# Kernel optimization log

Measured on AMD Instinct MI355X. Metric: run time of the kernel, lower is better.

The kernel has to match this reference:

```python
import jax, jax.numpy as jnp
import numpy as np

B, N, K = 8, 2048, 64          # clouds, points per cloud, max neighbors
R1, R2 = 0.2, 0.4              # radii of the two SA modules
S1, S2 = N // 2, N // 8        # fps: ratio 0.5, then 0.25 of S1
DIMS1 = [3, 64, 64, 128]
DIMS2 = [128 + 3, 128, 128, 256]
DIMS3 = [256 + 3, 256, 512, 1024]


def _fps(pos, S):
    # farthest point sampling, deterministic start at index 0. pos: [N,3] -> [S] int32
    d = jnp.sum((pos - pos[0]) ** 2, axis=-1)
    sel0 = jnp.zeros((S,), jnp.int32)
    def body(i, carry):
        d, sel = carry
        nxt = jnp.argmax(d).astype(jnp.int32)
        sel = sel.at[i].set(nxt)
        d = jnp.minimum(d, jnp.sum((pos - pos[nxt]) ** 2, axis=-1))
        return d, sel
    _, sel = jax.lax.fori_loop(1, S, body, (d, sel0))
    return sel


def _radius(c_pos, pos, r, k):
    # up to k nearest points within radius r of each centroid.
    d2 = jnp.sum((c_pos[:, None, :] - pos[None, :, :]) ** 2, axis=-1)  # [M,N]
    score = jnp.where(d2 <= r * r, -d2, -jnp.inf)
    neg, idx = jax.lax.top_k(score, k)   # nearest-first
    mask = neg > -jnp.inf
    return idx, mask


def _mlp(h, params):
    # PyG MLP, plain_last=True; BatchNorm at default init is identity -> omitted.
    n = len(params)
    for i, (W, b) in enumerate(params):
        h = h @ W + b
        if i < n - 1:
            h = jax.nn.relu(h)
    return h


def _sa(x, pos, S, r, params):
    # SAModule: fps -> radius -> PointNetConv (gather, per-edge MLP, max-aggregate)
    idx = _fps(pos, S)
    c_pos = pos[idx]                                  # [S,3]
    nbr, mask = _radius(c_pos, pos, r, K)             # [S,K]
    rel = pos[nbr] - c_pos[:, None, :]                # [S,K,3]
    h = rel if x is None else jnp.concatenate([x[nbr], rel], axis=-1)
    h = _mlp(h, params)                               # [S,K,C]
    # each centroid always contains itself in its ball, so no empty groups
    h = jnp.where(mask[:, :, None], h, -jnp.inf).max(axis=1)
    return h, c_pos


def _make_mlp_params(key, dims):
    params = []
    for i in range(len(dims) - 1):
        key, k1 = jax.random.split(key)
        W = jax.random.normal(k1, (dims[i], dims[i + 1]), jnp.float32) * np.sqrt(2.0 / dims[i])
        b = jnp.zeros((dims[i + 1],), jnp.float32)
        params += [W, b]
    return params, key


def setup_inputs() -> dict:
    key = jax.random.key(0)
    key, kp = jax.random.split(key)
    pos = jax.random.uniform(kp, (B, N, 3), jnp.float32)  # unit cube
    p1, key = _make_mlp_params(key, DIMS1)
    p2, key = _make_mlp_params(key, DIMS2)
    p3, key = _make_mlp_params(key, DIMS3)
    names1 = ['W1a', 'b1a', 'W1b', 'b1b', 'W1c', 'b1c']
    names2 = ['W2a', 'b2a', 'W2b', 'b2b', 'W2c', 'b2c']
    names3 = ['W3a', 'b3a', 'W3b', 'b3b', 'W3c', 'b3c']
    out = {'pos': pos}
    out.update(dict(zip(names1, p1)))
    out.update(dict(zip(names2, p2)))
    out.update(dict(zip(names3, p3)))
    return out


def reference(pos, W1a, b1a, W1b, b1b, W1c, b1c,
              W2a, b2a, W2b, b2b, W2c, b2c,
              W3a, b3a, W3b, b3b, W3c, b3c):
    params1 = [(W1a, b1a), (W1b, b1b), (W1c, b1c)]
    params2 = [(W2a, b2a), (W2b, b2b), (W2c, b2c)]
    params3 = [(W3a, b3a), (W3b, b3b), (W3c, b3c)]

    def per_cloud(p):
        h1, p1 = _sa(None, p, S1, R1, params1)        # [S1,128]
        h2, p2 = _sa(h1, p1, S2, R2, params2)         # [S2,256]
        g = _mlp(jnp.concatenate([h2, p2], axis=-1), params3)  # [S2,1024]
        return g.max(axis=0)                           # global max pool -> [1024]

    return jax.vmap(per_cloud)(pos)                    # [B,1024]
```

## Files before the change

kernel.cpp:

```cpp
#include <hip/hip_runtime.h>
#include <hip/hip_bf16.h>
#include <cstdint>
#include <cstddef>

#define B_CL   8
#define NPTS   2048
#define S1CNT  1024
#define S2CNT  256
#define KNBR   64

typedef unsigned short ushort;
typedef __attribute__((ext_vector_type(8))) short short8b;
typedef __attribute__((ext_vector_type(4))) float f32x4;

__device__ __forceinline__ ushort f2bf(float f) {
    union { __hip_bfloat16 h; ushort u; } v;
    v.h = __float2bfloat16(f);
    return v.u;
}
__device__ __forceinline__ float bf2f(ushort u) {
    return __uint_as_float(((unsigned)u) << 16);
}
__device__ __forceinline__ short8b ldfrag(const ushort* p) {
    return *(const short8b*)p;
}
__device__ __forceinline__ f32x4 mfma16(short8b a, short8b b, f32x4 c) {
    return __builtin_amdgcn_mfma_f32_16x16x32_bf16(a, b, c, 0, 0, 0);
}

__device__ __forceinline__ float dist2_exact(float ax, float ay, float az,
                                             float bx, float by, float bz) {
    float dx = __fsub_rn(ax, bx);
    float dy = __fsub_rn(ay, by);
    float dz = __fsub_rn(az, bz);
    return __fadd_rn(__fadd_rn(__fmul_rn(dx, dx), __fmul_rn(dy, dy)), __fmul_rn(dz, dz));
}

__device__ __forceinline__ unsigned long long wave_max_u64(unsigned long long k) {
#define DPP_STEP(CTRL) {                                                            \
    unsigned lo = (unsigned)k, hi = (unsigned)(k >> 32);                            \
    unsigned nlo = (unsigned)__builtin_amdgcn_update_dpp((int)lo, (int)lo, CTRL,    \
                                                         0xf, 0xf, false);          \
    unsigned nhi = (unsigned)__builtin_amdgcn_update_dpp((int)hi, (int)hi, CTRL,    \
                                                         0xf, 0xf, false);          \
    unsigned long long nk = ((unsigned long long)nhi << 32) | nlo;                  \
    if (nk > k) k = nk;                                                             \
}
    DPP_STEP(0x111);
    DPP_STEP(0x112);
    DPP_STEP(0x114);
    DPP_STEP(0x118);
    DPP_STEP(0x142);
    DPP_STEP(0x143);
#undef DPP_STEP
    return k;
}

template <int N, int S>
__global__ __launch_bounds__(256) void fps_kernel(const float* __restrict__ pos,
                                                  float* __restrict__ cpos) {
    constexpr int PPT = N / 256;
    __shared__ float px[N], py[N], pz[N];
    __shared__ float sel[S * 3];
    __shared__ unsigned long long kbuf[2][4];

    const int b   = blockIdx.x;
    const int tid = threadIdx.x;
    const float* P = pos + (size_t)b * N * 3;

    float ox[PPT], oy[PPT], oz[PPT], d[PPT];
    for (int j = 0; j < PPT; ++j) {
        int idx = tid + 256 * j;
        float x = P[idx * 3 + 0];
        float y = P[idx * 3 + 1];
        float z = P[idx * 3 + 2];
        px[idx] = x; py[idx] = y; pz[idx] = z;
        ox[j] = x; oy[j] = y; oz[j] = z;
        d[j] = 1e30f;
    }
    __syncthreads();

    float cx = px[0], cy = py[0], cz = pz[0];
    if (tid == 0) { sel[0] = cx; sel[1] = cy; sel[2] = cz; }

    for (int i = 1; i < S; ++i) {
        float bv = -1.0f;
        int   bi = 0;
        #pragma unroll
        for (int j = 0; j < PPT; ++j) {
            int idx = tid + 256 * j;
            float dd = dist2_exact(ox[j], oy[j], oz[j], cx, cy, cz);
            float nd = fminf(d[j], dd);
            d[j] = nd;
            if (nd > bv) { bv = nd; bi = idx; }
        }
        unsigned long long key =
            ((unsigned long long)__float_as_uint(bv) << 32) | (unsigned)(~bi);
        key = wave_max_u64(key);

        const int par = i & 1;
        if ((tid & 63) == 63) kbuf[par][tid >> 6] = key;
        __syncthreads();

        unsigned long long kk = kbuf[par][0];
        unsigned long long k1 = kbuf[par][1];
        unsigned long long k2 = kbuf[par][2];
        unsigned long long k3 = kbuf[par][3];
        if (k1 > kk) kk = k1;
        if (k2 > kk) kk = k2;
        if (k3 > kk) kk = k3;
        int nxt = (int)(~(unsigned)kk);

        cx = px[nxt]; cy = py[nxt]; cz = pz[nxt];
        if (tid == 0) {
            sel[i * 3 + 0] = cx;
            sel[i * 3 + 1] = cy;
            sel[i * 3 + 2] = cz;
        }
    }
    __syncthreads();
    float* cp = cpos + (size_t)b * S * 3;
    for (int j = tid; j < S * 3; j += 256) cp[j] = sel[j];
}

template <int N>
__global__ __launch_bounds__(256) void radius_kernel(const float* __restrict__ pos,
                                                     const float* __restrict__ cpos,
                                                     int M, float rr,
                                                     int* __restrict__ nbr,
                                                     int* __restrict__ cnt) {
    __shared__ unsigned long long list[N];
    __shared__ int c_sh;

    const int bm  = blockIdx.x;
    const int b   = bm / M;
    const int tid = threadIdx.x;
    const float* P = pos + (size_t)b * N * 3;

    const float cx = cpos[bm * 3 + 0];
    const float cy = cpos[bm * 3 + 1];
    const float cz = cpos[bm * 3 + 2];

    if (tid == 0) c_sh = 0;
    __syncthreads();

    for (int i = tid; i < N; i += 256) {
        float d2 = dist2_exact(cx, cy, cz, P[i * 3], P[i * 3 + 1], P[i * 3 + 2]);
        if (d2 <= rr) {
            int slot = atomicAdd(&c_sh, 1);
            list[slot] = ((unsigned long long)__float_as_uint(d2) << 32) | (unsigned int)i;
        }
    }
    __syncthreads();
    int C = c_sh;

    if (C <= KNBR) {
        if (tid < C) nbr[(size_t)bm * KNBR + tid] = (int)(list[tid] & 0xffffffffu);
        if (tid == 0) cnt[bm] = C;
        return;
    }

    int P2 = 1;
    while (P2 < C) P2 <<= 1;
    for (int i = C + tid; i < P2; i += 256) list[i] = ~0ULL;
    __syncthreads();
    for (int k = 2; k <= P2; k <<= 1) {
        for (int j = k >> 1; j > 0; j >>= 1) {
            for (int i = tid; i < P2; i += 256) {
                int l = i ^ j;
                if (l > i) {
                    unsigned long long a = list[i], bb = list[l];
                    bool up = ((i & k) == 0);
                    if ((a > bb) == up) { list[i] = bb; list[l] = a; }
                }
            }
            __syncthreads();
        }
    }
    if (tid < KNBR) nbr[(size_t)bm * KNBR + tid] = (int)(list[tid] & 0xffffffffu);
    if (tid == 0) cnt[bm] = KNBR;
}

__global__ __launch_bounds__(64) void wprep_kernel(const float* __restrict__ W,
                                                   ushort* __restrict__ Wt,
                                                   int K, int N, int Kpad) {
    const int n = blockIdx.x;
    for (int k = threadIdx.x; k < Kpad; k += 64)
        Wt[(size_t)n * Kpad + k] = (k < K) ? f2bf(W[(size_t)k * N + n]) : (ushort)0;
}

__global__ __launch_bounds__(256) void conv1_kernel(const float* __restrict__ pos,
                                                    const float* __restrict__ cpos,
                                                    const int* __restrict__ nbr,
                                                    const int* __restrict__ cnt,
                                                    const ushort* __restrict__ Wt1, const float* __restrict__ b1,
                                                    const ushort* __restrict__ Wt2, const float* __restrict__ b2,
                                                    const ushort* __restrict__ Wt3, const float* __restrict__ b3,
                                                    ushort* __restrict__ h1) {
    __shared__ ushort act1[64 * 72];
    __shared__ ushort act2[64 * 72];
    __shared__ int    snbr[KNBR];

    const int bm  = blockIdx.x;
    const int b   = bm >> 10;
    const int tid = threadIdx.x;
    const int C   = cnt[bm];

    const float cx = cpos[bm * 3 + 0];
    const float cy = cpos[bm * 3 + 1];
    const float cz = cpos[bm * 3 + 2];

    if (tid < KNBR) snbr[tid] = (tid < C) ? nbr[(size_t)bm * KNBR + tid] : 0;
    __syncthreads();

    const int lane = tid & 63, w = tid >> 6;
    const int lrow = lane & 15;
    const int lk8  = (lane >> 4) * 8;
    const int rbase = (lane >> 4) * 4;
    const f32x4 zz = {0.f, 0.f, 0.f, 0.f};

    short8b a0[4];
    #pragma unroll
    for (int mt = 0; mt < 4; ++mt) {
        short8b a = {0, 0, 0, 0, 0, 0, 0, 0};
        if (lane < 16) {
            const int nb = snbr[mt * 16 + lrow];
            const float* pp = pos + ((size_t)b * NPTS + nb) * 3;
            a[0] = (short)f2bf(pp[0] - cx);
            a[1] = (short)f2bf(pp[1] - cy);
            a[2] = (short)f2bf(pp[2] - cz);
        }
        a0[mt] = a;
    }

    {
        const int nt = w;
        short8b bf = ldfrag(Wt1 + (size_t)(nt * 16 + lrow) * 40 + lk8);
        const float bj = b1[nt * 16 + lrow];
        #pragma unroll
        for (int mt = 0; mt < 4; ++mt) {
            f32x4 acc = mfma16(a0[mt], bf, zz);
            #pragma unroll
            for (int r = 0; r < 4; ++r) {
                const int row = mt * 16 + rbase + r;
                act1[row * 72 + nt * 16 + lrow] = f2bf(fmaxf(acc[r] + bj, 0.f));
            }
        }
    }
    __syncthreads();

    {
        short8b af[4][2];
        #pragma unroll
        for (int mt = 0; mt < 4; ++mt)
            #pragma unroll
            for (int ks = 0; ks < 2; ++ks)
                af[mt][ks] = ldfrag(&act1[(mt * 16 + lrow) * 72 + ks * 32 + lk8]);
        const int nt = w;
        short8b bf0 = ldfrag(Wt2 + (size_t)(nt * 16 + lrow) * 72 + 0  + lk8);
        short8b bf1 = ldfrag(Wt2 + (size_t)(nt * 16 + lrow) * 72 + 32 + lk8);
        const float bj = b2[nt * 16 + lrow];
        #pragma unroll
        for (int mt = 0; mt < 4; ++mt) {
            f32x4 acc = mfma16(af[mt][0], bf0, zz);
            acc = mfma16(af[mt][1], bf1, acc);
            #pragma unroll
            for (int r = 0; r < 4; ++r) {
                const int row = mt * 16 + rbase + r;
                act2[row * 72 + nt * 16 + lrow] = f2bf(fmaxf(acc[r] + bj, 0.f));
            }
        }
    }
    __syncthreads();

    {
        short8b af[4][2];
        #pragma unroll
        for (int mt = 0; mt < 4; ++mt)
            #pragma unroll
            for (int ks = 0; ks < 2; ++ks)
                af[mt][ks] = ldfrag(&act2[(mt * 16 + lrow) * 72 + ks * 32 + lk8]);
        #pragma unroll
        for (int nti = 0; nti < 2; ++nti) {
            const int nt = w * 2 + nti;
            short8b bf0 = ldfrag(Wt3 + (size_t)(nt * 16 + lrow) * 72 + 0  + lk8);
            short8b bf1 = ldfrag(Wt3 + (size_t)(nt * 16 + lrow) * 72 + 32 + lk8);
            const float bj = b3[nt * 16 + lrow];
            float vm = -3.4e38f;
            #pragma unroll
            for (int mt = 0; mt < 4; ++mt) {
                f32x4 acc = mfma16(af[mt][0], bf0, zz);
                acc = mfma16(af[mt][1], bf1, acc);
                #pragma unroll
                for (int r = 0; r < 4; ++r) {
                    const int m = mt * 16 + rbase + r;
                    if (m < C) vm = fmaxf(vm, acc[r] + bj);
                }
            }
            vm = fmaxf(vm, __shfl_xor(vm, 16));
            vm = fmaxf(vm, __shfl_xor(vm, 32));
            if (lane < 16) h1[(size_t)bm * 128 + nt * 16 + lrow] = f2bf(vm);
        }
    }
}

__global__ __launch_bounds__(256) void conv2_kernel(const ushort* __restrict__ x,
                                                    const float* __restrict__ ppos,
                                                    const float* __restrict__ cpos,
                                                    const int* __restrict__ nbr,
                                                    const int* __restrict__ cnt,
                                                    const ushort* __restrict__ Wt1, const float* __restrict__ b1,
                                                    const ushort* __restrict__ Wt2, const float* __restrict__ b2,
                                                    const ushort* __restrict__ Wt3, const float* __restrict__ b3,
                                                    ushort* __restrict__ h2) {
    __shared__ ushort act0[64 * 168];
    __shared__ ushort act1[64 * 136];
    __shared__ int    snbr[KNBR];
    ushort* act2 = act0;

    const int bm  = blockIdx.x;
    const int b   = bm >> 8;
    const int tid = threadIdx.x;
    const int C   = cnt[bm];

    const float cx = cpos[bm * 3 + 0];
    const float cy = cpos[bm * 3 + 1];
    const float cz = cpos[bm * 3 + 2];

    if (tid < KNBR) snbr[tid] = (tid < C) ? nbr[(size_t)bm * KNBR + tid] : 0;
    __syncthreads();

    for (int e = tid; e < 1024; e += 256) {
        const int k = e >> 4, c = (e & 15) * 8;
        short8b v = {0, 0, 0, 0, 0, 0, 0, 0};
        if (k < C) v = ldfrag(x + ((size_t)b * S1CNT + snbr[k]) * 128 + c);
        *(short8b*)&act0[k * 168 + c] = v;
    }
    if (tid < KNBR) {
        const int k = tid;
        float r0 = 0.f, r1 = 0.f, r2 = 0.f;
        if (k < C) {
            const float* pp = ppos + ((size_t)b * S1CNT + snbr[k]) * 3;
            r0 = pp[0] - cx; r1 = pp[1] - cy; r2 = pp[2] - cz;
        }
        act0[k * 168 + 128] = f2bf(r0);
        act0[k * 168 + 129] = f2bf(r1);
        act0[k * 168 + 130] = f2bf(r2);
        for (int c = 131; c < 160; ++c) act0[k * 168 + c] = 0;
    }
    __syncthreads();

    const int lane = tid & 63, w = tid >> 6;
    const int lrow = lane & 15;
    const int lk8  = (lane >> 4) * 8;
    const int rbase = (lane >> 4) * 4;
    const f32x4 zz = {0.f, 0.f, 0.f, 0.f};

    {
        short8b af[4][5];
        #pragma unroll
        for (int mt = 0; mt < 4; ++mt)
            #pragma unroll
            for (int ks = 0; ks < 5; ++ks)
                af[mt][ks] = ldfrag(&act0[(mt * 16 + lrow) * 168 + ks * 32 + lk8]);
        #pragma unroll
        for (int nti = 0; nti < 2; ++nti) {
            const int nt = w * 2 + nti;
            f32x4 acc[4] = {zz, zz, zz, zz};
            #pragma unroll
            for (int ks = 0; ks < 5; ++ks) {
                short8b bf = ldfrag(Wt1 + (size_t)(nt * 16 + lrow) * 168 + ks * 32 + lk8);
                #pragma unroll
                for (int mt = 0; mt < 4; ++mt) acc[mt] = mfma16(af[mt][ks], bf, acc[mt]);
            }
            const float bj = b1[nt * 16 + lrow];
            #pragma unroll
            for (int mt = 0; mt < 4; ++mt)
                #pragma unroll
                for (int r = 0; r < 4; ++r) {
                    const int row = mt * 16 + rbase + r;
                    act1[row * 136 + nt * 16 + lrow] = f2bf(fmaxf(acc[mt][r] + bj, 0.f));
                }
        }
    }
    __syncthreads();

    {
        short8b af[4][4];
        #pragma unroll
        for (int mt = 0; mt < 4; ++mt)
            #pragma unroll
            for (int ks = 0; ks < 4; ++ks)
                af[mt][ks] = ldfrag(&act1[(mt * 16 + lrow) * 136 + ks * 32 + lk8]);
        #pragma unroll
        for (int nti = 0; nti < 2; ++nti) {
            const int nt = w * 2 + nti;
            f32x4 acc[4] = {zz, zz, zz, zz};
            #pragma unroll
            for (int ks = 0; ks < 4; ++ks) {
                short8b bf = ldfrag(Wt2 + (size_t)(nt * 16 + lrow) * 136 + ks * 32 + lk8);
                #pragma unroll
                for (int mt = 0; mt < 4; ++mt) acc[mt] = mfma16(af[mt][ks], bf, acc[mt]);
            }
            const float bj = b2[nt * 16 + lrow];
            #pragma unroll
            for (int mt = 0; mt < 4; ++mt)
                #pragma unroll
                for (int r = 0; r < 4; ++r) {
                    const int row = mt * 16 + rbase + r;
                    act2[row * 136 + nt * 16 + lrow] = f2bf(fmaxf(acc[mt][r] + bj, 0.f));
                }
        }
    }
    __syncthreads();

    {
        short8b af[4][4];
        #pragma unroll
        for (int mt = 0; mt < 4; ++mt)
            #pragma unroll
            for (int ks = 0; ks < 4; ++ks)
                af[mt][ks] = ldfrag(&act2[(mt * 16 + lrow) * 136 + ks * 32 + lk8]);
        #pragma unroll
        for (int nti = 0; nti < 4; ++nti) {
            const int nt = w * 4 + nti;
            f32x4 acc[4] = {zz, zz, zz, zz};
            #pragma unroll
            for (int ks = 0; ks < 4; ++ks) {
                short8b bf = ldfrag(Wt3 + (size_t)(nt * 16 + lrow) * 136 + ks * 32 + lk8);
                #pragma unroll
                for (int mt = 0; mt < 4; ++mt) acc[mt] = mfma16(af[mt][ks], bf, acc[mt]);
            }
            const float bj = b3[nt * 16 + lrow];
            float vm = -3.4e38f;
            #pragma unroll
            for (int mt = 0; mt < 4; ++mt)
                #pragma unroll
                for (int r = 0; r < 4; ++r) {
                    const int m = mt * 16 + rbase + r;
                    if (m < C) vm = fmaxf(vm, acc[mt][r] + bj);
                }
            vm = fmaxf(vm, __shfl_xor(vm, 16));
            vm = fmaxf(vm, __shfl_xor(vm, 32));
            if (lane < 16) h2[(size_t)bm * 256 + nt * 16 + lrow] = f2bf(vm);
        }
    }
}

__device__ __forceinline__ unsigned enc_f32(float f) {
    unsigned u = __float_as_uint(f);
    return (u & 0x80000000u) ? ~u : (u | 0x80000000u);
}

__global__ __launch_bounds__(256) void gmax_init_kernel(unsigned* __restrict__ gmax) {
    gmax[blockIdx.x * 256 + threadIdx.x] = 0u;
}

__global__ __launch_bounds__(256) void mlp3_kernel(const ushort* __restrict__ h2,
                                                   const float* __restrict__ cpos2,
                                                   const float* __restrict__ W1, const float* __restrict__ b1,
                                                   const float* __restrict__ W2, const float* __restrict__ b2,
                                                   const float* __restrict__ W3, const float* __restrict__ b3,
                                                   unsigned* __restrict__ gmax) {
    __shared__ float in4[4][260];
    __shared__ float a1s[4][256];
    __shared__ float a2s[4][512];

    const int bm0 = blockIdx.x * 4;
    const int bcl = bm0 >> 8;
    const int tid = threadIdx.x;

    #pragma unroll
    for (int r = 0; r < 4; ++r) {
        in4[r][tid] = bf2f(h2[(size_t)(bm0 + r) * 256 + tid]);
        if (tid < 3) in4[r][256 + tid] = cpos2[(bm0 + r) * 3 + tid];
    }
    __syncthreads();

    {
        const float bj = b1[tid];
        float acc[4] = {bj, bj, bj, bj};
        for (int i = 0; i < 259; ++i) {
            const float w = W1[i * 256 + tid];
            #pragma unroll
            for (int r = 0; r < 4; ++r) acc[r] += in4[r][i] * w;
        }
        #pragma unroll
        for (int r = 0; r < 4; ++r) a1s[r][tid] = fmaxf(acc[r], 0.f);
    }
    __syncthreads();

    {
        const float bj0 = b2[tid], bj1 = b2[tid + 256];
        float acc0[4] = {bj0, bj0, bj0, bj0};
        float acc1[4] = {bj1, bj1, bj1, bj1};
        for (int i = 0; i < 256; ++i) {
            const float w0 = W2[i * 512 + tid];
            const float w1 = W2[i * 512 + tid + 256];
            #pragma unroll
            for (int r = 0; r < 4; ++r) {
                const float a = a1s[r][i];
                acc0[r] += a * w0;
                acc1[r] += a * w1;
            }
        }
        #pragma unroll
        for (int r = 0; r < 4; ++r) {
            a2s[r][tid]       = fmaxf(acc0[r], 0.f);
            a2s[r][tid + 256] = fmaxf(acc1[r], 0.f);
        }
    }
    __syncthreads();

    {
        float acc[4][4];
        #pragma unroll
        for (int q = 0; q < 4; ++q) {
            const float bj = b3[tid + 256 * q];
            #pragma unroll
            for (int r = 0; r < 4; ++r) acc[q][r] = bj;
        }
        for (int i = 0; i < 512; ++i) {
            float av[4];
            #pragma unroll
            for (int r = 0; r < 4; ++r) av[r] = a2s[r][i];
            #pragma unroll
            for (int q = 0; q < 4; ++q) {
                const float w = W3[i * 1024 + 256 * q + tid];
                #pragma unroll
                for (int r = 0; r < 4; ++r) acc[q][r] += av[r] * w;
            }
        }
        #pragma unroll
        for (int q = 0; q < 4; ++q)
            #pragma unroll
            for (int r = 0; r < 4; ++r)
                atomicMax(&gmax[(size_t)bcl * 1024 + 256 * q + tid], enc_f32(acc[q][r]));
    }
}

__global__ __launch_bounds__(256) void gmax_decode_kernel(const unsigned* __restrict__ gmax,
                                                          float* __restrict__ out) {
    int t = blockIdx.x * 256 + threadIdx.x;
    unsigned u = gmax[t];
    out[t] = (u & 0x80000000u) ? __uint_as_float(u ^ 0x80000000u) : __uint_as_float(~u);
}

extern "C" void kernel_launch(void* const* d_in, const int* in_sizes, int n_in,
                              void* d_out, int out_size, void* d_ws, size_t ws_size,
                              hipStream_t stream) {
    (void)in_sizes; (void)n_in; (void)out_size; (void)ws_size;

    const float* pos = (const float*)d_in[0];
    const float* W1a = (const float*)d_in[1];  const float* b1a = (const float*)d_in[2];
    const float* W1b = (const float*)d_in[3];  const float* b1b = (const float*)d_in[4];
    const float* W1c = (const float*)d_in[5];  const float* b1c = (const float*)d_in[6];
    const float* W2a = (const float*)d_in[7];  const float* b2a = (const float*)d_in[8];
    const float* W2b = (const float*)d_in[9];  const float* b2b = (const float*)d_in[10];
    const float* W2c = (const float*)d_in[11]; const float* b2c = (const float*)d_in[12];
    const float* W3a = (const float*)d_in[13]; const float* b3a = (const float*)d_in[14];
    const float* W3b = (const float*)d_in[15]; const float* b3b = (const float*)d_in[16];
    const float* W3c = (const float*)d_in[17]; const float* b3c = (const float*)d_in[18];

    float* out = (float*)d_out;

    char* ws = (char*)d_ws;
    auto alloc = [&](size_t bytes) {
        char* p = ws;
        ws += (bytes + 255) & ~(size_t)255;
        return p;
    };
    float*    cpos1 = (float*)   alloc((size_t)B_CL * S1CNT * 3 * 4);
    int*      nbr1  = (int*)     alloc((size_t)B_CL * S1CNT * KNBR * 4);
    int*      cnt1  = (int*)     alloc((size_t)B_CL * S1CNT * 4);
    ushort*   h1    = (ushort*)  alloc((size_t)B_CL * S1CNT * 128 * 2);
    float*    cpos2 = (float*)   alloc((size_t)B_CL * S2CNT * 3 * 4);
    int*      nbr2  = (int*)     alloc((size_t)B_CL * S2CNT * KNBR * 4);
    int*      cnt2  = (int*)     alloc((size_t)B_CL * S2CNT * 4);
    ushort*   h2    = (ushort*)  alloc((size_t)B_CL * S2CNT * 256 * 2);
    unsigned* gmax  = (unsigned*)alloc((size_t)B_CL * 1024 * 4);
    ushort*   Wt1a  = (ushort*)  alloc((size_t)64  * 40  * 2);
    ushort*   Wt1b  = (ushort*)  alloc((size_t)64  * 72  * 2);
    ushort*   Wt1c  = (ushort*)  alloc((size_t)128 * 72  * 2);
    ushort*   Wt2a  = (ushort*)  alloc((size_t)128 * 168 * 2);
    ushort*   Wt2b  = (ushort*)  alloc((size_t)128 * 136 * 2);
    ushort*   Wt2c  = (ushort*)  alloc((size_t)256 * 136 * 2);

    const float RR1 = (float)(0.2 * 0.2);
    const float RR2 = (float)(0.4 * 0.4);

    wprep_kernel<<<64,  64, 0, stream>>>(W1a, Wt1a, 3,   64,  40);
    wprep_kernel<<<64,  64, 0, stream>>>(W1b, Wt1b, 64,  64,  72);
    wprep_kernel<<<128, 64, 0, stream>>>(W1c, Wt1c, 64,  128, 72);
    wprep_kernel<<<128, 64, 0, stream>>>(W2a, Wt2a, 131, 128, 168);
    wprep_kernel<<<128, 64, 0, stream>>>(W2b, Wt2b, 128, 128, 136);
    wprep_kernel<<<256, 64, 0, stream>>>(W2c, Wt2c, 128, 256, 136);

    fps_kernel<NPTS, S1CNT><<<B_CL, 256, 0, stream>>>(pos, cpos1);
    radius_kernel<NPTS><<<B_CL * S1CNT, 256, 0, stream>>>(pos, cpos1, S1CNT, RR1, nbr1, cnt1);
    conv1_kernel<<<B_CL * S1CNT, 256, 0, stream>>>(pos, cpos1, nbr1, cnt1,
                                                   Wt1a, b1a, Wt1b, b1b, Wt1c, b1c, h1);
    fps_kernel<S1CNT, S2CNT><<<B_CL, 256, 0, stream>>>(cpos1, cpos2);
    radius_kernel<S1CNT><<<B_CL * S2CNT, 256, 0, stream>>>(cpos1, cpos2, S2CNT, RR2, nbr2, cnt2);
    conv2_kernel<<<B_CL * S2CNT, 256, 0, stream>>>(h1, cpos1, cpos2, nbr2, cnt2,
                                                   Wt2a, b2a, Wt2b, b2b, Wt2c, b2c, h2);
    gmax_init_kernel<<<(B_CL * 1024) / 256, 256, 0, stream>>>(gmax);
    mlp3_kernel<<<(B_CL * S2CNT) / 4, 256, 0, stream>>>(h2, cpos2,
                                                        W3a, b3a, W3b, b3b, W3c, b3c, gmax);
    gmax_decode_kernel<<<(B_CL * 1024) / 256, 256, 0, stream>>>(gmax, out);
}
```

Before: 775.6 us.

## Batch two clouds per FPS block and overlap second FPS with radius search

```diff
diff --git a/kernel.cpp b/kernel.cpp
--- a/kernel.cpp
+++ b/kernel.cpp
@@ -56,83 +56,111 @@
     return k;
 }
 
-template <int N, int S>
+template <int N, int S, int CPB>
+__device__ __forceinline__ void fps_body(const float* __restrict__ pos,
+                                         float* __restrict__ cpos,
+                                         int b0, char* smem) {
+    constexpr int PPT = N / 256;
+    float* px = (float*)smem;
+    float* py = px + CPB * N;
+    float* pz = py + CPB * N;
+    unsigned long long* kbuf = (unsigned long long*)(pz + CPB * N);
+
+    const int tid = threadIdx.x;
+
+    float ox[CPB][PPT], oy[CPB][PPT], oz[CPB][PPT], d[CPB][PPT];
+    #pragma unroll
+    for (int c = 0; c < CPB; ++c) {
+        const float* P = pos + (size_t)(b0 + c) * N * 3;
+        #pragma unroll
+        for (int j = 0; j < PPT; ++j) {
+            int idx = tid + 256 * j;
+            float x = P[idx * 3 + 0];
+            float y = P[idx * 3 + 1];
+            float z = P[idx * 3 + 2];
+            px[c * N + idx] = x; py[c * N + idx] = y; pz[c * N + idx] = z;
+            ox[c][j] = x; oy[c][j] = y; oz[c][j] = z;
+            d[c][j] = 1e30f;
+        }
+    }
+    __syncthreads();
+
+    float cx[CPB], cy[CPB], cz[CPB];
+    #pragma unroll
+    for (int c = 0; c < CPB; ++c) {
+        cx[c] = px[c * N]; cy[c] = py[c * N]; cz[c] = pz[c * N];
+        if (tid == c * 64) {
+            float* cp = cpos + (size_t)(b0 + c) * S * 3;
+            cp[0] = cx[c]; cp[1] = cy[c]; cp[2] = cz[c];
+        }
+    }
+
+    for (int i = 1; i < S; ++i) {
+        unsigned long long key[CPB];
+        #pragma unroll
+        for (int c = 0; c < CPB; ++c) {
+            float bv = -1.0f;
+            int   bi = 0;
+            #pragma unroll
+            for (int j = 0; j < PPT; ++j) {
+                int idx = tid + 256 * j;
+                float dd = dist2_exact(ox[c][j], oy[c][j], oz[c][j], cx[c], cy[c], cz[c]);
+                float nd = fminf(d[c][j], dd);
+                d[c][j] = nd;
+                if (nd > bv) { bv = nd; bi = idx; }
+            }
+            key[c] = ((unsigned long long)__float_as_uint(bv) << 32) | (unsigned)(~bi);
+            key[c] = wave_max_u64(key[c]);
+        }
+
+        const int par = i & 1;
+        if ((tid & 63) == 63) {
+            #pragma unroll
+            for (int c = 0; c < CPB; ++c)
+                kbuf[(par * CPB + c) * 4 + (tid >> 6)] = key[c];
+        }
+        asm volatile("s_waitcnt lgkmcnt(0)" ::: "memory");
+        __builtin_amdgcn_s_barrier();
+        __builtin_amdgcn_sched_barrier(0);
+
+        #pragma unroll
+        for (int c = 0; c < CPB; ++c) {
+            unsigned long long kk = kbuf[(par * CPB + c) * 4 + 0];
+            unsigned long long k1 = kbuf[(par * CPB + c) * 4 + 1];
+            unsigned long long k2 = kbuf[(par * CPB + c) * 4 + 2];
+            unsigned long long k3 = kbuf[(par * CPB + c) * 4 + 3];
+            if (k1 > kk) kk = k1;
+            if (k2 > kk) kk = k2;
+            if (k3 > kk) kk = k3;
+            const int nxt = (int)(~(unsigned)kk);
+            cx[c] = px[c * N + nxt];
+            cy[c] = py[c * N + nxt];
+            cz[c] = pz[c * N + nxt];
+            if (tid == c * 64) {
+                float* cp = cpos + ((size_t)(b0 + c) * S + i) * 3;
+                cp[0] = cx[c]; cp[1] = cy[c]; cp[2] = cz[c];
+            }
+        }
+    }
+}
+
+template <int N, int S, int CPB>
 __global__ __launch_bounds__(256) void fps_kernel(const float* __restrict__ pos,
                                                   float* __restrict__ cpos) {
-    constexpr int PPT = N / 256;
-    __shared__ float px[N], py[N], pz[N];
-    __shared__ float sel[S * 3];
-    __shared__ unsigned long long kbuf[2][4];
-
-    const int b   = blockIdx.x;
-    const int tid = threadIdx.x;
-    const float* P = pos + (size_t)b * N * 3;
-
-    float ox[PPT], oy[PPT], oz[PPT], d[PPT];
-    for (int j = 0; j < PPT; ++j) {
-        int idx = tid + 256 * j;
-        float x = P[idx * 3 + 0];
-        float y = P[idx * 3 + 1];
-        float z = P[idx * 3 + 2];
-        px[idx] = x; py[idx] = y; pz[idx] = z;
-        ox[j] = x; oy[j] = y; oz[j] = z;
-        d[j] = 1e30f;
-    }
-    __syncthreads();
-
-    float cx = px[0], cy = py[0], cz = pz[0];
-    if (tid == 0) { sel[0] = cx; sel[1] = cy; sel[2] = cz; }
-
-    for (int i = 1; i < S; ++i) {
-        float bv = -1.0f;
-        int   bi = 0;
-        #pragma unroll
-        for (int j = 0; j < PPT; ++j) {
-            int idx = tid + 256 * j;
-            float dd = dist2_exact(ox[j], oy[j], oz[j], cx, cy, cz);
-            float nd = fminf(d[j], dd);
-            d[j] = nd;
-            if (nd > bv) { bv = nd; bi = idx; }
-        }
-        unsigned long long key =
-            ((unsigned long long)__float_as_uint(bv) << 32) | (unsigned)(~bi);
-        key = wave_max_u64(key);
-
-        const int par = i & 1;
-        if ((tid & 63) == 63) kbuf[par][tid >> 6] = key;
-        __syncthreads();
-
-        unsigned long long kk = kbuf[par][0];
-        unsigned long long k1 = kbuf[par][1];
-        unsigned long long k2 = kbuf[par][2];
-        unsigned long long k3 = kbuf[par][3];
-        if (k1 > kk) kk = k1;
-        if (k2 > kk) kk = k2;
-        if (k3 > kk) kk = k3;
-        int nxt = (int)(~(unsigned)kk);
-
-        cx = px[nxt]; cy = py[nxt]; cz = pz[nxt];
-        if (tid == 0) {
-            sel[i * 3 + 0] = cx;
-            sel[i * 3 + 1] = cy;
-            sel[i * 3 + 2] = cz;
-        }
-    }
-    __syncthreads();
-    float* cp = cpos + (size_t)b * S * 3;
-    for (int j = tid; j < S * 3; j += 256) cp[j] = sel[j];
+    __shared__ __align__(16) char smem[CPB * N * 3 * 4 + 2 * CPB * 4 * 8];
+    fps_body<N, S, CPB>(pos, cpos, blockIdx.x * CPB, smem);
 }
 
 template <int N>
-__global__ __launch_bounds__(256) void radius_kernel(const float* __restrict__ pos,
-                                                     const float* __restrict__ cpos,
-                                                     int M, float rr,
-                                                     int* __restrict__ nbr,
-                                                     int* __restrict__ cnt) {
-    __shared__ unsigned long long list[N];
-    __shared__ int c_sh;
-
-    const int bm  = blockIdx.x;
+__device__ __forceinline__ void radius_body(const float* __restrict__ pos,
+                                            const float* __restrict__ cpos,
+                                            int M, float rr,
+                                            int* __restrict__ nbr,
+                                            int* __restrict__ cnt,
+                                            char* smem, int bm) {
+    unsigned long long* list = (unsigned long long*)smem;
+    int* c_sh = (int*)(smem + (size_t)N * 8);
+
     const int b   = bm / M;
     const int tid = threadIdx.x;
     const float* P = pos + (size_t)b * N * 3;
@@ -141,18 +169,18 @@
     const float cy = cpos[bm * 3 + 1];
     const float cz = cpos[bm * 3 + 2];
 
-    if (tid == 0) c_sh = 0;
+    if (tid == 0) *c_sh = 0;
     __syncthreads();
 
     for (int i = tid; i < N; i += 256) {
         float d2 = dist2_exact(cx, cy, cz, P[i * 3], P[i * 3 + 1], P[i * 3 + 2]);
         if (d2 <= rr) {
-            int slot = atomicAdd(&c_sh, 1);
+            int slot = atomicAdd(c_sh, 1);
             list[slot] = ((unsigned long long)__float_as_uint(d2) << 32) | (unsigned int)i;
         }
     }
     __syncthreads();
-    int C = c_sh;
+    int C = *c_sh;
 
     if (C <= KNBR) {
         if (tid < C) nbr[(size_t)bm * KNBR + tid] = (int)(list[tid] & 0xffffffffu);
@@ -179,6 +207,32 @@
     }
     if (tid < KNBR) nbr[(size_t)bm * KNBR + tid] = (int)(list[tid] & 0xffffffffu);
     if (tid == 0) cnt[bm] = KNBR;
+}
+
+template <int N>
+__global__ __launch_bounds__(256) void radius_kernel(const float* __restrict__ pos,
+                                                     const float* __restrict__ cpos,
+                                                     int M, float rr,
+                                                     int* __restrict__ nbr,
+                                                     int* __restrict__ cnt) {
+    __shared__ __align__(16) char smem[(size_t)N * 8 + 16];
+    radius_body<N>(pos, cpos, M, rr, nbr, cnt, smem, blockIdx.x);
+}
+
+__global__ __launch_bounds__(256) void radius1_fps2_kernel(const float* __restrict__ pos,
+                                                           const float* __restrict__ cpos1,
+                                                           float rr1,
+                                                           int* __restrict__ nbr1,
+                                                           int* __restrict__ cnt1,
+                                                           float* __restrict__ cpos2) {
+    constexpr int    RB   = B_CL * S1CNT;
+    constexpr size_t SM_R = (size_t)NPTS * 8 + 16;
+    constexpr size_t SM_F = (size_t)2 * S1CNT * 3 * 4 + 2 * 2 * 4 * 8;
+    __shared__ __align__(16) char smem[SM_R > SM_F ? SM_R : SM_F];
+    if (blockIdx.x < RB)
+        radius_body<NPTS>(pos, cpos1, S1CNT, rr1, nbr1, cnt1, smem, blockIdx.x);
+    else
+        fps_body<S1CNT, S2CNT, 2>(cpos1, cpos2, (int)(blockIdx.x - RB) * 2, smem);
 }
 
 __global__ __launch_bounds__(64) void wprep_kernel(const float* __restrict__ W,
@@ -596,11 +650,11 @@
     wprep_kernel<<<128, 64, 0, stream>>>(W2b, Wt2b, 128, 128, 136);
     wprep_kernel<<<256, 64, 0, stream>>>(W2c, Wt2c, 128, 256, 136);
 
-    fps_kernel<NPTS, S1CNT><<<B_CL, 256, 0, stream>>>(pos, cpos1);
-    radius_kernel<NPTS><<<B_CL * S1CNT, 256, 0, stream>>>(pos, cpos1, S1CNT, RR1, nbr1, cnt1);
+    fps_kernel<NPTS, S1CNT, 2><<<B_CL / 2, 256, 0, stream>>>(pos, cpos1);
+    radius1_fps2_kernel<<<B_CL * S1CNT + B_CL / 2, 256, 0, stream>>>(pos, cpos1, RR1,
+                                                                     nbr1, cnt1, cpos2);
     conv1_kernel<<<B_CL * S1CNT, 256, 0, stream>>>(pos, cpos1, nbr1, cnt1,
                                                    Wt1a, b1a, Wt1b, b1b, Wt1c, b1c, h1);
-    fps_kernel<S1CNT, S2CNT><<<B_CL, 256, 0, stream>>>(cpos1, cpos2);
     radius_kernel<S1CNT><<<B_CL * S2CNT, 256, 0, stream>>>(cpos1, cpos2, S2CNT, RR2, nbr2, cnt2);
     conv2_kernel<<<B_CL * S2CNT, 256, 0, stream>>>(h1, cpos1, cpos2, nbr2, cnt2,
                                                    Wt2a, b2a, Wt2b, b2b, Wt2c, b2c, h2);
```

Measured after the change: 1.180 ms. 1.52x slower.
